# Kernel tuning notes

Hardware: AMD Instinct MI355X
Metric: run time of the kernel (lower is better)

Reference implementation:

```python
import jax, jax.numpy as jnp
import numpy as np

B, N, M = 4, 2048, 2048
DIM, DIM_KEYS, DIM_OUT = 512, 512, 512
HEADS, DIM_HEAD = 8, 64
INNER = HEADS * DIM_HEAD


def setup_inputs() -> dict:
    key = jax.random.key(0)
    ks = jax.random.split(key, 8)
    x = jax.random.normal(ks[0], (B, N, DIM), dtype=jnp.float32)
    context = jax.random.normal(ks[1], (B, M, DIM_KEYS), dtype=jnp.float32)
    Wq = jax.random.normal(ks[2], (DIM, INNER), dtype=jnp.float32) / np.sqrt(DIM)
    Wkv = jax.random.normal(ks[3], (DIM_KEYS, 2 * INNER), dtype=jnp.float32) / np.sqrt(DIM_KEYS)
    null_k = jax.random.normal(ks[4], (DIM_HEAD,), dtype=jnp.float32)
    null_v = jax.random.normal(ks[5], (DIM_HEAD,), dtype=jnp.float32)
    Wout = jax.random.normal(ks[6], (INNER, DIM_OUT), dtype=jnp.float32) / np.sqrt(INNER)
    bout = jnp.zeros((DIM_OUT,), dtype=jnp.float32)
    return {"x": x, "context": context, "Wq": Wq, "Wkv": Wkv,
            "null_k": null_k, "null_v": null_v, "Wout": Wout, "bout": bout}


def reference(x, context, Wq, Wkv, null_k, null_v, Wout, bout):
    b = x.shape[0]
    scale = DIM_HEAD ** (-0.5)
    q = x @ Wq                      # [b, n, inner]
    kv = context @ Wkv              # [b, m, 2*inner]
    k, v = jnp.split(kv, 2, axis=-1)
    # [b, h, n, d]
    q = q.reshape(b, -1, HEADS, DIM_HEAD).transpose(0, 2, 1, 3)
    k = k.reshape(b, -1, HEADS, DIM_HEAD).transpose(0, 2, 1, 3)
    v = v.reshape(b, -1, HEADS, DIM_HEAD).transpose(0, 2, 1, 3)
    # prepend null key/value token: [b, h, 1, d]
    nk = jnp.broadcast_to(null_k, (b, HEADS, 1, DIM_HEAD))
    nv = jnp.broadcast_to(null_v, (b, HEADS, 1, DIM_HEAD))
    k = jnp.concatenate((nk, k), axis=-2)  # [b, h, m+1, d]
    v = jnp.concatenate((nv, v), axis=-2)
    q = jnp.tanh(q)
    k = jnp.tanh(k)
    sim = jnp.einsum('bhid,bhjd->bhij', q, k) * scale  # [b, h, n, m+1]
    attn = jax.nn.softmax(sim, axis=-1)
    out = jnp.einsum('bhij,bhjd->bhid', attn, v)       # [b, h, n, d]
    out = out.transpose(0, 2, 1, 3).reshape(b, -1, INNER)  # [b, n, inner]
    return out @ Wout + bout
```

## Files before the change

### kernel.cpp

```cpp
#include <hip/hip_runtime.h>
#include <hip/hip_bf16.h>
#include <stdint.h>

#define B_    4
#define N_    2048
#define M_    2048
#define DIMX  512
#define INNER 512
#define H_    8
#define DH    64
#define MK    2049
#define MKP   2112

#define QSCALE  0.18033688011f
#define SM_BIAS -11.5415605f

using u16 = unsigned short;
using u32 = unsigned int;

typedef __attribute__((ext_vector_type(8))) short short8;
typedef __attribute__((ext_vector_type(4))) float f32x4;

#if defined(__has_builtin)
# if __has_builtin(__builtin_amdgcn_exp2f)
#  define EXP2(x) __builtin_amdgcn_exp2f(x)
# endif
#endif
#ifndef EXP2
# define EXP2(x) exp2f(x)
#endif

__device__ __forceinline__ u16 bfc(float f){
  __hip_bfloat16 h = __float2bfloat16(f);
  return *reinterpret_cast<u16*>(&h);
}
__device__ __forceinline__ u32 bfpk(float lo, float hi){
  return (u32)bfc(lo) | ((u32)bfc(hi) << 16);
}

__global__ __launch_bounds__(256) void convert_bf(
    const float* __restrict__ x, const float* __restrict__ ctx,
    u16* __restrict__ xb, u16* __restrict__ cb)
{
  const float* in = blockIdx.z ? ctx : x;
  u16* out        = blockIdx.z ? cb : xb;
  const int i = blockIdx.x * 256 + threadIdx.x;
  float4 a = ((const float4*)in)[i*2];
  float4 b = ((const float4*)in)[i*2+1];
  uint4 t;
  t.x = bfpk(a.x, a.y); t.y = bfpk(a.z, a.w);
  t.z = bfpk(b.x, b.y); t.w = bfpk(b.z, b.w);
  ((uint4*)out)[i] = t;
}

__global__ __launch_bounds__(256) void transpose_all(
    const float* __restrict__ Wq, const float* __restrict__ Wkv,
    const float* __restrict__ Wout,
    u16* __restrict__ Wqt, u16* __restrict__ Wkvt, u16* __restrict__ Woutt)
{
  const int z = blockIdx.z;
  const float* in = (z == 0) ? Wq : (z == 1) ? Wkv : Wout;
  u16* out        = (z == 0) ? Wqt : (z == 1) ? Wkvt : Woutt;
  const int C     = (z == 1) ? 1024 : 512;
  const int R     = 512;
  if (blockIdx.x * 64 >= C) return;

  __shared__ float tl[64][65];
  const int t = threadIdx.x;
  const int c0 = blockIdx.x * 64, r0 = blockIdx.y * 64;
  const int col = t & 63, rb = t >> 6;
  #pragma unroll
  for (int j = 0; j < 16; ++j){
    const int row = rb + j*4;
    tl[row][col] = in[(size_t)(r0 + row) * C + c0 + col];
  }
  __syncthreads();
  #pragma unroll
  for (int j = 0; j < 16; ++j){
    const int orow = rb + j*4;
    out[(size_t)(c0 + orow) * R + r0 + col] = bfc(tl[col][orow]);
  }
}

#define PROJ_COMPUTE(bi)                                                      \
  {                                                                           \
    short8 af[4], bf[4];                                                      \
    _Pragma("unroll")                                                         \
    for (int m = 0; m < 4; ++m){                                              \
      const int row = wr + m*16 + c;                                          \
      af[m] = *(const short8*)((char*)At[bi] + row*64 + ((g ^ ((row>>1)&3)) << 4)); \
    }                                                                         \
    _Pragma("unroll")                                                         \
    for (int n = 0; n < 4; ++n){                                              \
      const int row = wc + n*16 + c;                                          \
      bf[n] = *(const short8*)((char*)Bl[bi] + row*64 + ((g ^ ((row>>1)&3)) << 4)); \
    }                                                                         \
    __builtin_amdgcn_s_setprio(1);                                            \
    _Pragma("unroll")                                                         \
    for (int m = 0; m < 4; ++m)                                               \
      _Pragma("unroll")                                                       \
      for (int n = 0; n < 4; ++n)                                             \
        acc[m][n] = __builtin_amdgcn_mfma_f32_16x16x32_bf16(af[m], bf[n], acc[m][n], 0, 0, 0); \
    __builtin_amdgcn_s_setprio(0);                                            \
  }

__global__ __launch_bounds__(256, 3) void fused_proj(
    const u16* __restrict__ xb, const u16* __restrict__ cb,
    const u16* __restrict__ Wqt, const u16* __restrict__ Wkvt,
    u16* __restrict__ qb, u16* __restrict__ kb, u16* __restrict__ vb)
{
  __shared__ __align__(16) short At[2][128*32];
  __shared__ __align__(16) short Bl[2][128*32];

  const int flat = blockIdx.x;
  const int tile = (flat & 7) * 96 + (flat >> 3);
  const bool isq = tile < 256;
  const int lt   = isq ? tile : tile - 256;
  const int gx   = isq ? 4 : 8;
  const int row0 = (lt / gx) * 128, col0 = (lt % gx) * 128;
  const u16* A  = isq ? xb : cb;
  const u16* Bt = isq ? Wqt : Wkvt;

  const int tid = threadIdx.x;
  const int w = tid >> 6, lane = tid & 63;
  const int c = lane & 15, g = lane >> 4;
  const int wr = (w >> 1) * 64, wc = (w & 1) * 64;

  f32x4 acc[4][4] = {};

  const int srow = tid >> 1, sj = (tid & 1) * 2;
  const int swz0 = ((sj  ) ^ ((srow >> 1) & 3)) << 4;
  const int swz1 = ((sj+1) ^ ((srow >> 1) & 3)) << 4;

  const u16* asrc = A  + (size_t)(row0 + srow) * DIMX + sj*8;
  const u16* bsrc = Bt + (size_t)(col0 + srow) * DIMX + sj*8;

  uint4 aA0, aA1, bA0, bA1;
  uint4 aB0, aB1, bB0, bB1;

  aA0 = ((const uint4*)asrc)[0];        aA1 = ((const uint4*)asrc)[1];
  bA0 = ((const uint4*)bsrc)[0];        bA1 = ((const uint4*)bsrc)[1];
  aB0 = ((const uint4*)(asrc + 32))[0]; aB1 = ((const uint4*)(asrc + 32))[1];
  bB0 = ((const uint4*)(bsrc + 32))[0]; bB1 = ((const uint4*)(bsrc + 32))[1];
  *(uint4*)((char*)At[0] + srow*64 + swz0) = aA0;
  *(uint4*)((char*)At[0] + srow*64 + swz1) = aA1;
  *(uint4*)((char*)Bl[0] + srow*64 + swz0) = bA0;
  *(uint4*)((char*)Bl[0] + srow*64 + swz1) = bA1;

  for (int kk = 0; kk < 16; kk += 2){
    __syncthreads();
    if (kk + 2 < 16){
      const u16* an = asrc + (kk+2)*32;
      const u16* bn = bsrc + (kk+2)*32;
      aA0 = ((const uint4*)an)[0]; aA1 = ((const uint4*)an)[1];
      bA0 = ((const uint4*)bn)[0]; bA1 = ((const uint4*)bn)[1];
    }
    PROJ_COMPUTE(0);
    *(uint4*)((char*)At[1] + srow*64 + swz0) = aB0;
    *(uint4*)((char*)At[1] + srow*64 + swz1) = aB1;
    *(uint4*)((char*)Bl[1] + srow*64 + swz0) = bB0;
    *(uint4*)((char*)Bl[1] + srow*64 + swz1) = bB1;

    __syncthreads();
    if (kk + 3 < 16){
      const u16* an = asrc + (kk+3)*32;
      const u16* bn = bsrc + (kk+3)*32;
      aB0 = ((const uint4*)an)[0]; aB1 = ((const uint4*)an)[1];
      bB0 = ((const uint4*)bn)[0]; bB1 = ((const uint4*)bn)[1];
    }
    PROJ_COMPUTE(1);
    if (kk + 2 < 16){
      *(uint4*)((char*)At[0] + srow*64 + swz0) = aA0;
      *(uint4*)((char*)At[0] + srow*64 + swz1) = aA1;
      *(uint4*)((char*)Bl[0] + srow*64 + swz0) = bA0;
      *(uint4*)((char*)Bl[0] + srow*64 + swz1) = bA1;
    }
  }

  #pragma unroll
  for (int m = 0; m < 4; ++m){
    #pragma unroll
    for (int n = 0; n < 4; ++n){
      #pragma unroll
      for (int rr = 0; rr < 4; ++rr){
        const int R = row0 + wr + m*16 + g*4 + rr;
        const int col = col0 + wc + n*16 + c;
        const float v = acc[m][n][rr];
        if (isq){
          qb[(size_t)R * INNER + col] = bfc(tanhf(v) * QSCALE);
        } else {
          const int bidx = R >> 11, mm = R & 2047;
          if (col < INNER){
            const int h = col >> 6, d = col & 63;
            kb[((size_t)(bidx*H_ + h) * MKP + (mm + 1)) * DH + d] = bfc(tanhf(v));
          } else {
            const int cc = col - INNER;
            const int h = cc >> 6, d = cc & 63;
            vb[((size_t)(bidx*H_ + h) * MKP + (mm + 1)) * DH + d] = bfc(v);
          }
        }
      }
    }
  }
}

__global__ __launch_bounds__(256, 3) void mgemm_out(
    const u16* __restrict__ A, const u16* __restrict__ Bt,
    float* __restrict__ Cf, const float* __restrict__ bias)
{
  __shared__ __align__(16) short At[2][128*32];
  __shared__ __align__(16) short Bl[2][128*32];

  const int flat = blockIdx.x;
  const int tile = (flat & 7) * 32 + (flat >> 3);
  const int row0 = (tile >> 2) * 128, col0 = (tile & 3) * 128;

  const int tid = threadIdx.x;
  const int w = tid >> 6, lane = tid & 63;
  const int c = lane & 15, g = lane >> 4;
  const int wr = (w >> 1) * 64, wc = (w & 1) * 64;

  f32x4 acc[4][4] = {};

  const int srow = tid >> 1, sj = (tid & 1) * 2;
  const int swz0 = ((sj  ) ^ ((srow >> 1) & 3)) << 4;
  const int swz1 = ((sj+1) ^ ((srow >> 1) & 3)) << 4;

  const u16* asrc = A  + (size_t)(row0 + srow) * INNER + sj*8;
  const u16* bsrc = Bt + (size_t)(col0 + srow) * INNER + sj*8;

  uint4 aA0, aA1, bA0, bA1;
  uint4 aB0, aB1, bB0, bB1;

  aA0 = ((const uint4*)asrc)[0];        aA1 = ((const uint4*)asrc)[1];
  bA0 = ((const uint4*)bsrc)[0];        bA1 = ((const uint4*)bsrc)[1];
  aB0 = ((const uint4*)(asrc + 32))[0]; aB1 = ((const uint4*)(asrc + 32))[1];
  bB0 = ((const uint4*)(bsrc + 32))[0]; bB1 = ((const uint4*)(bsrc + 32))[1];
  *(uint4*)((char*)At[0] + srow*64 + swz0) = aA0;
  *(uint4*)((char*)At[0] + srow*64 + swz1) = aA1;
  *(uint4*)((char*)Bl[0] + srow*64 + swz0) = bA0;
  *(uint4*)((char*)Bl[0] + srow*64 + swz1) = bA1;

  for (int kk = 0; kk < 16; kk += 2){
    __syncthreads();
    if (kk + 2 < 16){
      const u16* an = asrc + (kk+2)*32;
      const u16* bn = bsrc + (kk+2)*32;
      aA0 = ((const uint4*)an)[0]; aA1 = ((const uint4*)an)[1];
      bA0 = ((const uint4*)bn)[0]; bA1 = ((const uint4*)bn)[1];
    }
    PROJ_COMPUTE(0);
    *(uint4*)((char*)At[1] + srow*64 + swz0) = aB0;
    *(uint4*)((char*)At[1] + srow*64 + swz1) = aB1;
    *(uint4*)((char*)Bl[1] + srow*64 + swz0) = bB0;
    *(uint4*)((char*)Bl[1] + srow*64 + swz1) = bB1;

    __syncthreads();
    if (kk + 3 < 16){
      const u16* an = asrc + (kk+3)*32;
      const u16* bn = bsrc + (kk+3)*32;
      aB0 = ((const uint4*)an)[0]; aB1 = ((const uint4*)an)[1];
      bB0 = ((const uint4*)bn)[0]; bB1 = ((const uint4*)bn)[1];
    }
    PROJ_COMPUTE(1);
    if (kk + 2 < 16){
      *(uint4*)((char*)At[0] + srow*64 + swz0) = aA0;
      *(uint4*)((char*)At[0] + srow*64 + swz1) = aA1;
      *(uint4*)((char*)Bl[0] + srow*64 + swz0) = bA0;
      *(uint4*)((char*)Bl[0] + srow*64 + swz1) = bA1;
    }
  }

  #pragma unroll
  for (int m = 0; m < 4; ++m){
    #pragma unroll
    for (int n = 0; n < 4; ++n){
      #pragma unroll
      for (int rr = 0; rr < 4; ++rr){
        const int R = row0 + wr + m*16 + g*4 + rr;
        const int col = col0 + wc + n*16 + c;
        Cf[(size_t)R * 512 + col] = acc[m][n][rr] + bias[col];
      }
    }
  }
}

__global__ __launch_bounds__(256) void vtrans(
    const u16* __restrict__ vb, u16* __restrict__ vt,
    const float* __restrict__ nk, const float* __restrict__ nv,
    u16* __restrict__ kb)
{
  __shared__ short tl[64][72];
  const int t = threadIdx.x;
  const int mt = blockIdx.x, bh = blockIdx.y;
  {
    const int mr = t >> 2, chb = (t & 3) * 2;
    const u16* src = vb + ((size_t)bh * MKP + mt*64 + mr) * DH + chb*8;
    uint4 a = ((const uint4*)src)[0];
    uint4 b = ((const uint4*)src)[1];
    *(uint4*)((char*)tl + mr*144 + chb*16)     = a;
    *(uint4*)((char*)tl + mr*144 + (chb+1)*16) = b;
  }
  __syncthreads();
  {
    const int d = t >> 2, chb = (t & 3) * 2;
    #pragma unroll
    for (int j = 0; j < 2; ++j){
      const int mbase = (chb + j) * 8;
      u16 s[8];
      #pragma unroll
      for (int e = 0; e < 8; ++e) s[e] = (u16)tl[mbase + e][d];
      if (mt == 0 && mbase == 0) s[0] = bfc(nv[d]);
      uint4 o;
      o.x = (u32)s[0] | ((u32)s[1] << 16);
      o.y = (u32)s[2] | ((u32)s[3] << 16);
      o.z = (u32)s[4] | ((u32)s[5] << 16);
      o.w = (u32)s[6] | ((u32)s[7] << 16);
      *(uint4*)(vt + ((size_t)bh * DH + d) * MKP + mt*64 + mbase) = o;
    }
    if (mt == 0 && (t & 3) == 0)
      kb[(size_t)bh * MKP * DH + d] = bfc(tanhf(nk[d]));
  }
}

__global__ __launch_bounds__(256) void attn_mfma(
    const u16* __restrict__ qb, const u16* __restrict__ kb,
    const u16* __restrict__ vt, u16* __restrict__ aob)
{
  __shared__ __align__(16) short Kl[2][64*64];
  __shared__ __align__(16) short Vl[2][64*64];
  __shared__ __align__(16) short Pl[4][32*64];

  const int tid  = threadIdx.x;
  const int w    = tid >> 6;
  const int lane = tid & 63;
  const int c    = lane & 15;
  const int g    = lane >> 4;
  const int bh   = blockIdx.y, b = bh >> 3, h = bh & 7;
  const int qbase = blockIdx.x * 128 + w * 32;
  const int xr   = (c & 7) << 4;

  short8 qf[2][2];
  #pragma unroll
  for (int u = 0; u < 2; ++u){
    const u16* qrow = qb + ((size_t)(b*N_) + qbase + u*16 + c) * INNER + h * DH;
    qf[u][0] = *(const short8*)(qrow + g*8);
    qf[u][1] = *(const short8*)(qrow + 32 + g*8);
  }

  f32x4 o[2][4] = {};
  float l0 = 0.f, l1 = 0.f;

  const u16* kbase = kb + (size_t)bh * MKP * DH;
  const u16* vbase = vt + (size_t)bh * DH * MKP;
  const int srow = tid >> 2, sch = (tid & 3) * 2;
  const int swz0 = ((sch  ) ^ (srow & 7)) << 4;
  const int swz1 = ((sch+1) ^ (srow & 7)) << 4;

  uint4 rk0, rk1, rv0, rv1;
  {
    const u16* ksrc = kbase + (size_t)srow * DH + sch*8;
    rk0 = ((const uint4*)ksrc)[0]; rk1 = ((const uint4*)ksrc)[1];
    const u16* vsrc = vbase + (size_t)srow * MKP + sch*8;
    rv0 = ((const uint4*)vsrc)[0]; rv1 = ((const uint4*)vsrc)[1];
  }
  *(uint4*)((char*)Kl[0] + srow*128 + swz0) = rk0;
  *(uint4*)((char*)Kl[0] + srow*128 + swz1) = rk1;
  *(uint4*)((char*)Vl[0] + srow*128 + swz0) = rv0;
  *(uint4*)((char*)Vl[0] + srow*128 + swz1) = rv1;

  int cur = 0;
  for (int kt = 0; kt < 33; ++kt){
    __syncthreads();
    if (kt < 32){
      const u16* ksrc = kbase + (size_t)((kt+1)*64 + srow) * DH + sch*8;
      rk0 = ((const uint4*)ksrc)[0]; rk1 = ((const uint4*)ksrc)[1];
      const u16* vsrc = vbase + (size_t)srow * MKP + (kt+1)*64 + sch*8;
      rv0 = ((const uint4*)vsrc)[0]; rv1 = ((const uint4*)vsrc)[1];
    }

    const char* Kc = (const char*)Kl[cur];
    const char* Vc = (const char*)Vl[cur];
    char*       Pw = (char*)Pl + w*4096;

    f32x4 sv[2][4];
    __builtin_amdgcn_s_setprio(1);
    #pragma unroll
    for (int s = 0; s < 4; ++s){
      const int row = s*16 + c;
      short8 kf0 = *(const short8*)(Kc + row*128 + ((     g*16) ^ xr));
      short8 kf1 = *(const short8*)(Kc + row*128 + ((64 + g*16) ^ xr));
      f32x4 a0 = {SM_BIAS, SM_BIAS, SM_BIAS, SM_BIAS};
      f32x4 a1 = {SM_BIAS, SM_BIAS, SM_BIAS, SM_BIAS};
      a0 = __builtin_amdgcn_mfma_f32_16x16x32_bf16(kf0, qf[0][0], a0, 0, 0, 0);
      a1 = __builtin_amdgcn_mfma_f32_16x16x32_bf16(kf0, qf[1][0], a1, 0, 0, 0);
      a0 = __builtin_amdgcn_mfma_f32_16x16x32_bf16(kf1, qf[0][1], a0, 0, 0, 0);
      a1 = __builtin_amdgcn_mfma_f32_16x16x32_bf16(kf1, qf[1][1], a1, 0, 0, 0);
      sv[0][s] = a0; sv[1][s] = a1;
    }
    __builtin_amdgcn_s_setprio(0);

    if (kt == 32){
      #pragma unroll
      for (int u = 0; u < 2; ++u)
        #pragma unroll
        for (int s = 0; s < 4; ++s)
          #pragma unroll
          for (int r = 0; r < 4; ++r)
            if (s | r) sv[u][s][r] = -1e30f;
      if (g){ sv[0][0][0] = -1e30f; sv[1][0][0] = -1e30f; }
    }

    #pragma unroll
    for (int u = 0; u < 2; ++u){
      float psum = 0.f;
      #pragma unroll
      for (int s = 0; s < 4; ++s){
        const float p0 = EXP2(sv[u][s][0]);
        const float p1 = EXP2(sv[u][s][1]);
        const float p2 = EXP2(sv[u][s][2]);
        const float p3 = EXP2(sv[u][s][3]);
        psum += (p0 + p1) + (p2 + p3);
        uint2 pk;
        pk.x = bfpk(p0, p1);
        pk.y = bfpk(p2, p3);
        *(uint2*)(Pw + (u*16 + c)*128
                  + ((((2*s + (g>>1)) ^ (c&7)) << 4) | ((g&1)*8))) = pk;
      }
      psum += __shfl_xor(psum, 16);
      psum += __shfl_xor(psum, 32);
      if (u == 0) l0 += psum; else l1 += psum;
    }

    __builtin_amdgcn_s_setprio(1);
    #pragma unroll
    for (int hh = 0; hh < 2; ++hh){
      short8 pf0 = *(const short8*)(Pw + (     c)*128 + (((hh*4 + g) ^ (c&7)) << 4));
      short8 pf1 = *(const short8*)(Pw + (16 + c)*128 + (((hh*4 + g) ^ (c&7)) << 4));
      #pragma unroll
      for (int D = 0; D < 4; ++D){
        short8 vf = *(const short8*)(Vc + (D*16 + c)*128 + ((hh*64 + g*16) ^ xr));
        o[0][D] = __builtin_amdgcn_mfma_f32_16x16x32_bf16(pf0, vf, o[0][D], 0, 0, 0);
        o[1][D] = __builtin_amdgcn_mfma_f32_16x16x32_bf16(pf1, vf, o[1][D], 0, 0, 0);
      }
    }
    __builtin_amdgcn_s_setprio(0);

    if (kt < 32){
      char* Kn = (char*)Kl[cur ^ 1];
      char* Vn = (char*)Vl[cur ^ 1];
      *(uint4*)(Kn + srow*128 + swz0) = rk0;
      *(uint4*)(Kn + srow*128 + swz1) = rk1;
      *(uint4*)(Vn + srow*128 + swz0) = rv0;
      *(uint4*)(Vn + srow*128 + swz1) = rv1;
      cur ^= 1;
    }
  }

  #pragma unroll
  for (int u = 0; u < 2; ++u){
    const float inv = 1.f / (u ? l1 : l0);
    #pragma unroll
    for (int r = 0; r < 4; ++r){
      const float ir = __shfl(inv, g*4 + r, 16);
      const size_t nrow = (size_t)(b*N_) + qbase + u*16 + g*4 + r;
      #pragma unroll
      for (int D = 0; D < 4; ++D)
        aob[nrow * INNER + h*DH + D*16 + c] = bfc(o[u][D][r] * ir);
    }
  }
}

extern "C" void kernel_launch(void* const* d_in, const int* in_sizes, int n_in,
                              void* d_out, int out_size, void* d_ws, size_t ws_size,
                              hipStream_t stream)
{
  const float* x    = (const float*)d_in[0];
  const float* ctx  = (const float*)d_in[1];
  const float* Wq   = (const float*)d_in[2];
  const float* Wkv  = (const float*)d_in[3];
  const float* nk   = (const float*)d_in[4];
  const float* nv   = (const float*)d_in[5];
  const float* Wout = (const float*)d_in[6];
  const float* bout = (const float*)d_in[7];
  float* out = (float*)d_out;

  char* ws = (char*)d_ws;
  u16* xb    = (u16*)(ws);
  u16* cb    = (u16*)(ws +  8388608);
  u16* qb    = (u16*)(ws + 16777216);
  u16* kbB   = (u16*)(ws + 25165824);
  u16* vbB   = (u16*)(ws + 33816576);
  u16* vtb   = (u16*)(ws + 42467328);
  u16* Wqt   = (u16*)(ws + 51118080);
  u16* Wkvt  = (u16*)(ws + 51642368);
  u16* Woutt = (u16*)(ws + 52690944);
  u16* aoB   = vbB;

  convert_bf<<<dim3(2048, 1, 2), 256, 0, stream>>>(x, ctx, xb, cb);
  transpose_all<<<dim3(16, 8, 3), 256, 0, stream>>>(Wq, Wkv, Wout, Wqt, Wkvt, Woutt);

  fused_proj<<<768, 256, 0, stream>>>(xb, cb, Wqt, Wkvt, qb, kbB, vbB);
  vtrans<<<dim3(33, 32), 256, 0, stream>>>(vbB, vtb, nk, nv, kbB);
  attn_mfma<<<dim3(16, 32), 256, 0, stream>>>(qb, kbB, vtb, aoB);
  mgemm_out<<<256, 256, 0, stream>>>(aoB, Woutt, out, bout);
}
```

Baseline: 113.9 us.

## Split attention over key dimension into three chunks and add combine kernel

Attention now splits the 33 key tiles into three chunks of 11 via a third grid dimension. Each chunk writes unnormalized bf16 partial outputs and row sums, and a new combine kernel adds them and normalizes. The old grid had only 512 blocks on a GPU with 256 CUs, so this is meant to raise occupancy and balance the load. The cost is an extra launch, extra partial-output traffic, and partials rounded to bf16 before the reduction. That works only because softmax uses a fixed bias instead of a running max.

Result: slower. 124.6 us (+9.4%).

```diff
diff --git a/kernel.cpp b/kernel.cpp
--- a/kernel.cpp
+++ b/kernel.cpp
@@ -36,6 +36,9 @@
 }
 __device__ __forceinline__ u32 bfpk(float lo, float hi){
   return (u32)bfc(lo) | ((u32)bfc(hi) << 16);
+}
+__device__ __forceinline__ float bf2f(u32 u){
+  union { u32 u; float f; } x; x.u = u << 16; return x.f;
 }
 
 __global__ __launch_bounds__(256) void convert_bf(
@@ -325,7 +328,7 @@
 
 __global__ __launch_bounds__(256) void attn_mfma(
     const u16* __restrict__ qb, const u16* __restrict__ kb,
-    const u16* __restrict__ vt, u16* __restrict__ aob)
+    const u16* __restrict__ vt, u16* __restrict__ po, float* __restrict__ pl)
 {
   __shared__ __align__(16) short Kl[2][64*64];
   __shared__ __align__(16) short Vl[2][64*64];
@@ -337,6 +340,8 @@
   const int c    = lane & 15;
   const int g    = lane >> 4;
   const int bh   = blockIdx.y, b = bh >> 3, h = bh & 7;
+  const int z    = blockIdx.z;
+  const int kt0  = z * 11;
   const int qbase = blockIdx.x * 128 + w * 32;
   const int xr   = (c & 7) << 4;
 
@@ -359,9 +364,9 @@
 
   uint4 rk0, rk1, rv0, rv1;
   {
-    const u16* ksrc = kbase + (size_t)srow * DH + sch*8;
+    const u16* ksrc = kbase + (size_t)(kt0*64 + srow) * DH + sch*8;
     rk0 = ((const uint4*)ksrc)[0]; rk1 = ((const uint4*)ksrc)[1];
-    const u16* vsrc = vbase + (size_t)srow * MKP + sch*8;
+    const u16* vsrc = vbase + (size_t)srow * MKP + kt0*64 + sch*8;
     rv0 = ((const uint4*)vsrc)[0]; rv1 = ((const uint4*)vsrc)[1];
   }
   *(uint4*)((char*)Kl[0] + srow*128 + swz0) = rk0;
@@ -370,9 +375,10 @@
   *(uint4*)((char*)Vl[0] + srow*128 + swz1) = rv1;
 
   int cur = 0;
-  for (int kt = 0; kt < 33; ++kt){
+  for (int kl = 0; kl < 11; ++kl){
+    const int kt = kt0 + kl;
     __syncthreads();
-    if (kt < 32){
+    if (kl < 10){
       const u16* ksrc = kbase + (size_t)((kt+1)*64 + srow) * DH + sch*8;
       rk0 = ((const uint4*)ksrc)[0]; rk1 = ((const uint4*)ksrc)[1];
       const u16* vsrc = vbase + (size_t)srow * MKP + (kt+1)*64 + sch*8;
@@ -446,7 +452,7 @@
     }
     __builtin_amdgcn_s_setprio(0);
 
-    if (kt < 32){
+    if (kl < 10){
       char* Kn = (char*)Kl[cur ^ 1];
       char* Vn = (char*)Vl[cur ^ 1];
       *(uint4*)(Kn + srow*128 + swz0) = rk0;
@@ -457,18 +463,46 @@
     }
   }
 
+  const size_t prow0 = (size_t)(z*32 + bh) * 2048 + qbase;
   #pragma unroll
   for (int u = 0; u < 2; ++u){
-    const float inv = 1.f / (u ? l1 : l0);
     #pragma unroll
     for (int r = 0; r < 4; ++r){
-      const float ir = __shfl(inv, g*4 + r, 16);
-      const size_t nrow = (size_t)(b*N_) + qbase + u*16 + g*4 + r;
+      const size_t prow = prow0 + u*16 + g*4 + r;
       #pragma unroll
       for (int D = 0; D < 4; ++D)
-        aob[nrow * INNER + h*DH + D*16 + c] = bfc(o[u][D][r] * ir);
-    }
-  }
+        po[prow*64 + D*16 + c] = bfc(o[u][D][r]);
+    }
+  }
+  if (g == 0){
+    pl[prow0 + c]      = l0;
+    pl[prow0 + 16 + c] = l1;
+  }
+}
+
+__global__ __launch_bounds__(256) void combine(
+    const u16* __restrict__ po, const float* __restrict__ pl,
+    u16* __restrict__ ao)
+{
+  const int gidx = blockIdx.x * 256 + threadIdx.x;
+  const int ri = gidx >> 4;
+  const int dq = (gidx & 15) * 4;
+  const int bh = ri >> 11, n = ri & 2047;
+  const int b = bh >> 3, h = bh & 7;
+
+  const float L = pl[ri] + pl[65536 + ri] + pl[131072 + ri];
+  float s0 = 0.f, s1 = 0.f, s2 = 0.f, s3 = 0.f;
+  #pragma unroll
+  for (int z = 0; z < 3; ++z){
+    uint2 t = *(const uint2*)(po + ((size_t)z*65536 + ri)*64 + dq);
+    s0 += bf2f(t.x & 0xffffu); s1 += bf2f(t.x >> 16);
+    s2 += bf2f(t.y & 0xffffu); s3 += bf2f(t.y >> 16);
+  }
+  const float inv = 1.f / L;
+  uint2 o;
+  o.x = bfpk(s0 * inv, s1 * inv);
+  o.y = bfpk(s2 * inv, s3 * inv);
+  *(uint2*)(ao + ((size_t)(b*N_ + n)) * INNER + h*DH + dq) = o;
 }
 
 extern "C" void kernel_launch(void* const* d_in, const int* in_sizes, int n_in,
@@ -486,22 +520,25 @@
   float* out = (float*)d_out;
 
   char* ws = (char*)d_ws;
-  u16* xb    = (u16*)(ws);
-  u16* cb    = (u16*)(ws +  8388608);
-  u16* qb    = (u16*)(ws + 16777216);
-  u16* kbB   = (u16*)(ws + 25165824);
-  u16* vbB   = (u16*)(ws + 33816576);
-  u16* vtb   = (u16*)(ws + 42467328);
-  u16* Wqt   = (u16*)(ws + 51118080);
-  u16* Wkvt  = (u16*)(ws + 51642368);
-  u16* Woutt = (u16*)(ws + 52690944);
-  u16* aoB   = vbB;
+  u16*   xb    = (u16*)(ws);
+  u16*   cb    = (u16*)(ws +  8388608);
+  u16*   vbB   = (u16*)(ws + 16777216);
+  u16*   po    = (u16*)(ws);
+  float* pl    = (float*)(ws + 25427968);
+  u16*   qb    = (u16*)(ws + 26214400);
+  u16*   kbB   = (u16*)(ws + 34603008);
+  u16*   vtb   = (u16*)(ws + 43253760);
+  u16*   Wqt   = (u16*)(ws + 51904512);
+  u16*   Wkvt  = (u16*)(ws + 52428800);
+  u16*   Woutt = (u16*)(ws + 53477376);
+  u16*   aoB   = (u16*)(ws + 54001664);
 
   convert_bf<<<dim3(2048, 1, 2), 256, 0, stream>>>(x, ctx, xb, cb);
   transpose_all<<<dim3(16, 8, 3), 256, 0, stream>>>(Wq, Wkv, Wout, Wqt, Wkvt, Woutt);
 
   fused_proj<<<768, 256, 0, stream>>>(xb, cb, Wqt, Wkvt, qb, kbB, vbB);
   vtrans<<<dim3(33, 32), 256, 0, stream>>>(vbB, vtb, nk, nv, kbB);
-  attn_mfma<<<dim3(16, 32), 256, 0, stream>>>(qb, kbB, vtb, aoB);
+  attn_mfma<<<dim3(16, 32, 3), 256, 0, stream>>>(qb, kbB, vtb, po, pl);
+  combine<<<4096, 256, 0, stream>>>(po, pl, aoB);
   mgemm_out<<<256, 256, 0, stream>>>(aoB, Woutt, out, bout);
 }
```
